# Kernel tuning notes

Hardware: AMD Instinct MI355X
Metric: run time of the kernel (lower is better)

Reference implementation:

```python
import jax, jax.numpy as jnp
import numpy as np

EPS_FEAT = 1e-4   # stabilizer eps inside favorp_projection
EPS_DEN = 0.01    # clamp_min eps for the attention denominator


def favorp_projection(data, projection_matrix, is_query):
    # data: [b, h, n, d]; projection_matrix: [h, m, d]
    d = data.shape[-1]
    data_normalizer = d ** (-0.25)
    ratio = projection_matrix.shape[1] ** (-0.5)
    data_dash = jnp.einsum('bhnd,hmd->bhnm', data_normalizer * data, projection_matrix)
    diag_data = (jnp.sum(data * data, axis=-1) * 0.5 * data_normalizer * data_normalizer)[..., None]
    if is_query:
        stabilizer = jax.lax.stop_gradient(jnp.max(data_dash, axis=-1, keepdims=True))
    else:
        stabilizer = jax.lax.stop_gradient(jnp.max(data_dash, axis=(-1, -2), keepdims=True))
    return ratio * jnp.exp(data_dash - diag_data - stabilizer) + EPS_FEAT


def setup_inputs() -> dict:
    key = jax.random.key(0)
    ks = jax.random.split(key, 12)
    N, B, E, H, D, M = 4096, 4, 1024, 16, 64, 64
    s = E ** -0.5
    return {
        'query': jax.random.normal(ks[0], (N, B, E), jnp.float32),
        'key': jax.random.normal(ks[1], (N, B, E), jnp.float32),
        'value': jax.random.normal(ks[2], (N, B, E), jnp.float32),
        'Wq': jax.random.normal(ks[3], (E, E), jnp.float32) * s,
        'bq': jax.random.normal(ks[4], (E,), jnp.float32) * 0.02,
        'Wk': jax.random.normal(ks[5], (E, E), jnp.float32) * s,
        'bk': jax.random.normal(ks[6], (E,), jnp.float32) * 0.02,
        'Wv': jax.random.normal(ks[7], (E, E), jnp.float32) * s,
        'bv': jax.random.normal(ks[8], (E,), jnp.float32) * 0.02,
        'Wo': jax.random.normal(ks[9], (E, E), jnp.float32) * s,
        'bo': jax.random.normal(ks[10], (E,), jnp.float32) * 0.02,
        'proj': jax.random.normal(ks[11], (H, M, D), jnp.float32),
    }


def reference(query, key, value, Wq, bq, Wk, bk, Wv, bv, Wo, bo, proj):
    H = proj.shape[0]
    # [n, b, e] -> [b, n, e]
    q_in = query.transpose(1, 0, 2)
    k_in = key.transpose(1, 0, 2)
    v_in = value.transpose(1, 0, 2)
    B, N, E = q_in.shape
    D = E // H

    def lin(x, W, b):
        return jnp.einsum('bne,fe->bnf', x, W) + b

    def split_heads(x):  # [b, n, e] -> [b, h, n, d]
        return x.reshape(B, N, H, D).transpose(0, 2, 1, 3)

    q = split_heads(lin(q_in, Wq, bq))
    k = split_heads(lin(k_in, Wk, bk))
    v = split_heads(lin(v_in, Wv, bv))

    q_prime = favorp_projection(q, proj, is_query=True)   # [b, h, n, m]
    k_prime = favorp_projection(k, proj, is_query=False)  # [b, h, n, m]

    # non-causal linear attention: O(n * m * d)
    kv = jnp.einsum('bhnm,bhnd->bhmd', k_prime, v)
    qkv = jnp.einsum('bhnm,bhmd->bhnd', q_prime, kv)
    normalizer = jnp.einsum('bhnm,bhm->bhn', q_prime, k_prime.sum(axis=2))
    output = qkv / jnp.maximum(normalizer[..., None], EPS_DEN)

    attn_output = output.transpose(0, 2, 1, 3).reshape(B, N, E)  # b h n d -> b n (h d)
    out = lin(attn_output, Wo, bo)
    return out.transpose(1, 0, 2)  # back to [n, b, e]
```

## Files before the change

kernel.cpp:

```cpp
#include <hip/hip_runtime.h>
#include <math.h>

#define B_   4
#define N_   4096
#define E_   1024
#define H_   16
#define BN_  (B_*N_)
#define BH_  (B_*H_)
#define SPLITK 8

#define NRM_C   0.35355339059327373f
#define DIAG_C  0.0625f
#define RATIO_C 0.125f
#define EPSF    1e-4f
#define EPSD    0.01f

typedef __attribute__((ext_vector_type(8))) short bf16x8;
typedef __attribute__((ext_vector_type(4))) float f32x4;

__device__ __forceinline__ unsigned short f32_to_bf16(float x) {
    unsigned int u = __float_as_uint(x);
    unsigned int r = (u + 0x7fffu + ((u >> 16) & 1u)) >> 16;
    return (unsigned short)r;
}
__device__ __forceinline__ float bf16_to_f32(unsigned short h) {
    return __uint_as_float(((unsigned int)h) << 16);
}

__device__ __forceinline__ unsigned int pk_bf16(float a, float b) {
    unsigned int r;
    asm("v_cvt_pk_bf16_f32 %0, %1, %2" : "=v"(r) : "v"(a), "v"(b));
    return r;
}

__device__ __forceinline__ void f32x8_split(float4 fa, float4 fb, bf16x8& hi, bf16x8& lo) {
    unsigned int h0 = pk_bf16(fa.x, fa.y), h1 = pk_bf16(fa.z, fa.w);
    unsigned int h2 = pk_bf16(fb.x, fb.y), h3 = pk_bf16(fb.z, fb.w);
    float e0 = __uint_as_float(h0 << 16), e1 = __uint_as_float(h0 & 0xffff0000u);
    float e2 = __uint_as_float(h1 << 16), e3 = __uint_as_float(h1 & 0xffff0000u);
    float e4 = __uint_as_float(h2 << 16), e5 = __uint_as_float(h2 & 0xffff0000u);
    float e6 = __uint_as_float(h3 << 16), e7 = __uint_as_float(h3 & 0xffff0000u);
    unsigned int l0 = pk_bf16(fa.x - e0, fa.y - e1), l1 = pk_bf16(fa.z - e2, fa.w - e3);
    unsigned int l2 = pk_bf16(fb.x - e4, fb.y - e5), l3 = pk_bf16(fb.z - e6, fb.w - e7);
    union { unsigned int u[4]; bf16x8 v; } H, L;
    H.u[0] = h0; H.u[1] = h1; H.u[2] = h2; H.u[3] = h3;
    L.u[0] = l0; L.u[1] = l1; L.u[2] = l2; L.u[3] = l3;
    hi = H.v; lo = L.v;
}

__device__ __forceinline__ void atomicMaxF(float* addr, float v) {
    if (v >= 0.f) atomicMax((int*)addr, __float_as_int(v));
    else          atomicMin((unsigned int*)addr, __float_as_uint(v));
}

__global__ void init_stab(float* stab) {
    if (threadIdx.x < BH_) stab[threadIdx.x] = -INFINITY;
}

template<int IN_MODE>
__global__ __launch_bounds__(256) void convert_split(const float* __restrict__ src,
                                                     unsigned short* __restrict__ hi,
                                                     unsigned short* __restrict__ lo,
                                                     int total4)
{
    int i = blockIdx.x * 256 + threadIdx.x;
    const int stride = gridDim.x * 256;
    for (; i < total4; i += stride) {
        long e4 = (long)i * 4;
        const float* p;
        if (IN_MODE == 0) {
            long r = e4 >> 10; int e = (int)(e4 & 1023);
            int b = (int)(r >> 12), n = (int)(r & 4095);
            p = src + (((long)(n * B_ + b)) << 10) + e;
        } else {
            p = src + e4;
        }
        float4 v = *(const float4*)p;
        ushort4 h, l;
        h.x = f32_to_bf16(v.x); l.x = f32_to_bf16(v.x - bf16_to_f32(h.x));
        h.y = f32_to_bf16(v.y); l.y = f32_to_bf16(v.y - bf16_to_f32(h.y));
        h.z = f32_to_bf16(v.z); l.z = f32_to_bf16(v.z - bf16_to_f32(h.z));
        h.w = f32_to_bf16(v.w); l.w = f32_to_bf16(v.w - bf16_to_f32(h.w));
        *(ushort4*)(hi + e4) = h;
        *(ushort4*)(lo + e4) = l;
    }
}

__device__ __forceinline__ void gl_lds16(const unsigned short* g, unsigned short* l) {
    __builtin_amdgcn_global_load_lds((const __attribute__((address_space(1))) void*)g,
                                     (__attribute__((address_space(3))) void*)l, 16, 0, 0);
}

#define SMEM_BYTES (4*64*68*4 + 2*4*64*4)

template<int MODE>
__global__ __launch_bounds__(256) void gemm_mfma(const unsigned short* __restrict__ Ahi,
                                                 const unsigned short* __restrict__ Alo,
                                                 const unsigned short* __restrict__ Bhi,
                                                 const unsigned short* __restrict__ Blo,
                                                 const float* __restrict__ bias,
                                                 float* __restrict__ Y,
                                                 float* __restrict__ stab,
                                                 const unsigned short* __restrict__ PShi,
                                                 const unsigned short* __restrict__ PSlo,
                                                 const unsigned short* __restrict__ kvThi,
                                                 const unsigned short* __restrict__ kvTlo,
                                                 const float* __restrict__ ksum,
                                                 unsigned short* __restrict__ AttnHi,
                                                 unsigned short* __restrict__ AttnLo)
{
    __shared__ __align__(16) char SMEM[SMEM_BYTES];
    unsigned short* smem = (unsigned short*)SMEM;
    const int t = threadIdx.x;
    const int w = t >> 6, lane = t & 63;
    const int row0 = blockIdx.x * 128, col0 = blockIdx.y * 128;
    const int wrow = (w >> 1) * 64, wcol = (w & 1) * 64;
    const int g = lane >> 4, rl = lane & 15;
    const int lr8 = lane >> 3, lc8 = lane & 7;

    const int sr = w * 32 + (lane >> 2);
    const int kswz = (((lane & 3) ^ ((lane >> 2) & 3)) << 3);
    const long aoff = (long)(row0 + sr) * E_ + kswz;
    const long boff = (long)(col0 + sr) * E_ + kswz;

    f32x4 acc[4][4];
#pragma unroll
    for (int m = 0; m < 4; ++m)
#pragma unroll
        for (int n = 0; n < 4; ++n) acc[m][n] = (f32x4){0.f, 0.f, 0.f, 0.f};

#define STAGE_STEP(KS, BUF)                                                          \
    {                                                                                \
        const int k0 = (KS) * 32;                                                    \
        unsigned short* d = smem + (BUF) * 16384 + w * 1024;                         \
        gl_lds16(Ahi + aoff + k0,             d);                                    \
        gl_lds16(Ahi + aoff + k0 + 16 * E_,   d + 512);                              \
        gl_lds16(Alo + aoff + k0,             d + 4096);                             \
        gl_lds16(Alo + aoff + k0 + 16 * E_,   d + 4096 + 512);                       \
        gl_lds16(Bhi + boff + k0,             d + 8192);                             \
        gl_lds16(Bhi + boff + k0 + 16 * E_,   d + 8192 + 512);                       \
        gl_lds16(Blo + boff + k0,             d + 12288);                            \
        gl_lds16(Blo + boff + k0 + 16 * E_,   d + 12288 + 512);                      \
    }

    STAGE_STEP(0, 0);

    for (int ks = 0; ks < 32; ++ks) {
        __syncthreads();
        if (ks + 1 < 32) STAGE_STEP(ks + 1, (ks + 1) & 1);
        const unsigned short* sb = smem + (ks & 1) * 16384;
        bf16x8 ah[4], al[4], bh[4], bl[4];
#pragma unroll
        for (int m = 0; m < 4; ++m) {
            int r = wrow + m * 16 + rl;
            int off = r * 32 + ((g ^ (r & 3)) << 3);
            ah[m] = *(const bf16x8*)(sb + off);
            al[m] = *(const bf16x8*)(sb + 4096 + off);
        }
#pragma unroll
        for (int n = 0; n < 4; ++n) {
            int r = wcol + n * 16 + rl;
            int off = r * 32 + ((g ^ (r & 3)) << 3);
            bh[n] = *(const bf16x8*)(sb + 8192 + off);
            bl[n] = *(const bf16x8*)(sb + 12288 + off);
        }
#pragma unroll
        for (int m = 0; m < 4; ++m)
#pragma unroll
            for (int n = 0; n < 4; ++n)
                acc[m][n] = __builtin_amdgcn_mfma_f32_16x16x32_bf16(ah[m], bh[n], acc[m][n], 0, 0, 0);
#pragma unroll
        for (int m = 0; m < 4; ++m)
#pragma unroll
            for (int n = 0; n < 4; ++n)
                acc[m][n] = __builtin_amdgcn_mfma_f32_16x16x32_bf16(ah[m], bl[n], acc[m][n], 0, 0, 0);
#pragma unroll
        for (int m = 0; m < 4; ++m)
#pragma unroll
            for (int n = 0; n < 4; ++n)
                acc[m][n] = __builtin_amdgcn_mfma_f32_16x16x32_bf16(al[m], bh[n], acc[m][n], 0, 0, 0);
    }
#undef STAGE_STEP

    float bv[4];
#pragma unroll
    for (int n = 0; n < 4; ++n) bv[n] = bias[col0 + wcol + n * 16 + rl];

    if (MODE <= 1) {
#pragma unroll
        for (int m = 0; m < 4; ++m) {
            int rbase = row0 + wrow + m * 16 + g * 4;
#pragma unroll
            for (int n = 0; n < 4; ++n) {
                int c = col0 + wcol + n * 16 + rl;
#pragma unroll
                for (int q = 0; q < 4; ++q) {
                    int r = rbase + q;
                    float v = acc[m][n][q] + bv[n];
                    long off;
                    if (MODE == 0) off = (long)r * E_ + c;
                    else { int b = r >> 12, nn = r & (N_ - 1); off = (long)(nn * B_ + b) * E_ + c; }
                    Y[off] = v;
                }
            }
        }
        return;
    }

    __syncthreads();
    float* accF  = (float*)SMEM + w * (64 * 68);
    float* diagL = (float*)(SMEM + 4*64*68*4) + w * 64;
    float* rnmL  = (float*)(SMEM + 4*64*68*4) + 256 + w * 64;
    const int b_idx = row0 >> 12;
    const int hg = (col0 >> 6) + (w & 1);
    const int bh_i = b_idx * H_ + hg;

    bf16x8 pbh[8], pbl[8];
#pragma unroll
    for (int n = 0; n < 4; ++n)
#pragma unroll
        for (int kk = 0; kk < 2; ++kk) {
            long po = (long)hg * 4096 + (n*16 + rl) * 64 + kk*32 + g*8;
            pbh[n*2+kk] = *(const bf16x8*)(PShi + po);
            pbl[n*2+kk] = *(const bf16x8*)(PSlo + po);
        }

#pragma unroll
    for (int m = 0; m < 4; ++m)
#pragma unroll
        for (int n = 0; n < 4; ++n)
#pragma unroll
            for (int q = 0; q < 4; ++q)
                accF[(m*16 + g*4 + q) * 68 + n*16 + rl] = acc[m][n][q] + bv[n];
    {
        float s = 0.f;
#pragma unroll 16
        for (int d = 0; d < 64; ++d) { float x = accF[lane * 68 + d]; s = fmaf(x, x, s); }
        diagL[lane] = s * DIAG_C;
    }
    __syncthreads();

    float wavemax = -INFINITY;
#pragma unroll
    for (int mi = 0; mi < 4; ++mi) {
        bf16x8 dah[2], dal[2];
#pragma unroll
        for (int kk = 0; kk < 2; ++kk) {
            const float* src = &accF[(mi*16 + rl) * 68 + kk*32 + g*8];
            float4 f0 = *(const float4*)src, f1 = *(const float4*)(src + 4);
            f32x8_split(f0, f1, dah[kk], dal[kk]);
        }
        f32x4 dacc[4];
#pragma unroll
        for (int n = 0; n < 4; ++n) dacc[n] = (f32x4){0.f,0.f,0.f,0.f};
#pragma unroll
        for (int n = 0; n < 4; ++n)
#pragma unroll
            for (int kk = 0; kk < 2; ++kk) {
                dacc[n] = __builtin_amdgcn_mfma_f32_16x16x32_bf16(dah[kk], pbh[n*2+kk], dacc[n], 0, 0, 0);
                dacc[n] = __builtin_amdgcn_mfma_f32_16x16x32_bf16(dah[kk], pbl[n*2+kk], dacc[n], 0, 0, 0);
                dacc[n] = __builtin_amdgcn_mfma_f32_16x16x32_bf16(dal[kk], pbh[n*2+kk], dacc[n], 0, 0, 0);
            }
        if (MODE == 2) {
#pragma unroll
            for (int n = 0; n < 4; ++n)
#pragma unroll
                for (int q = 0; q < 4; ++q) {
                    float dsh = dacc[n][q] * NRM_C;
                    wavemax = fmaxf(wavemax, dsh);
                    int rloc = mi*16 + g*4 + q;
                    accF[rloc * 68 + n*16 + rl] = dsh - diagL[rloc];
                }
        } else {
            float rm0 = -INFINITY, rm1 = -INFINITY, rm2 = -INFINITY, rm3 = -INFINITY;
#pragma unroll
            for (int n = 0; n < 4; ++n) {
                rm0 = fmaxf(rm0, dacc[n][0]); rm1 = fmaxf(rm1, dacc[n][1]);
                rm2 = fmaxf(rm2, dacc[n][2]); rm3 = fmaxf(rm3, dacc[n][3]);
            }
#pragma unroll
            for (int off = 1; off < 16; off <<= 1) {
                rm0 = fmaxf(rm0, __shfl_xor(rm0, off));
                rm1 = fmaxf(rm1, __shfl_xor(rm1, off));
                rm2 = fmaxf(rm2, __shfl_xor(rm2, off));
                rm3 = fmaxf(rm3, __shfl_xor(rm3, off));
            }
            float rmq[4] = {rm0 * NRM_C, rm1 * NRM_C, rm2 * NRM_C, rm3 * NRM_C};
#pragma unroll
            for (int n = 0; n < 4; ++n)
#pragma unroll
                for (int q = 0; q < 4; ++q) {
                    int rloc = mi*16 + g*4 + q;
                    float qp = RATIO_C * expf(dacc[n][q] * NRM_C - diagL[rloc] - rmq[q]) + EPSF;
                    accF[rloc * 68 + n*16 + rl] = qp;
                }
        }
    }

    if (MODE == 2) {
#pragma unroll
        for (int off = 1; off < 64; off <<= 1) wavemax = fmaxf(wavemax, __shfl_xor(wavemax, off));
        if (lane == 0) atomicMaxF(&stab[bh_i], wavemax);
#pragma unroll
        for (int pass = 0; pass < 8; ++pass) {
            int rloc = pass * 8 + lr8;
            const float* sp = &accF[rloc * 68 + lc8 * 8];
            float4 f0 = *(const float4*)sp;
            float4 f1 = *(const float4*)(sp + 4);
            long off = (long)(row0 + wrow + rloc) * E_ + col0 + wcol + lc8 * 8;
            *(float4*)(Y + off) = f0;
            *(float4*)(Y + off + 4) = f1;
        }
        return;
    }

    {
        float s = 0.f;
        const float* kb = ksum + bh_i * 64;
#pragma unroll 16
        for (int m = 0; m < 64; ++m) s = fmaf(accF[lane * 68 + m], kb[m], s);
        rnmL[lane] = 1.f / fmaxf(s, EPSD);
    }
    bf16x8 kbh[8], kbl[8];
#pragma unroll
    for (int n = 0; n < 4; ++n)
#pragma unroll
        for (int kk = 0; kk < 2; ++kk) {
            long ko = (long)bh_i * 4096 + (n*16 + rl) * 64 + kk*32 + g*8;
            kbh[n*2+kk] = *(const bf16x8*)(kvThi + ko);
            kbl[n*2+kk] = *(const bf16x8*)(kvTlo + ko);
        }
    __syncthreads();
#pragma unroll
    for (int mi = 0; mi < 4; ++mi) {
        bf16x8 qah[2], qal[2];
#pragma unroll
        for (int kk = 0; kk < 2; ++kk) {
            const float* src = &accF[(mi*16 + rl) * 68 + kk*32 + g*8];
            float4 f0 = *(const float4*)src, f1 = *(const float4*)(src + 4);
            f32x8_split(f0, f1, qah[kk], qal[kk]);
        }
        f32x4 oacc[4];
#pragma unroll
        for (int n = 0; n < 4; ++n) oacc[n] = (f32x4){0.f,0.f,0.f,0.f};
#pragma unroll
        for (int n = 0; n < 4; ++n)
#pragma unroll
            for (int kk = 0; kk < 2; ++kk) {
                oacc[n] = __builtin_amdgcn_mfma_f32_16x16x32_bf16(qah[kk], kbh[n*2+kk], oacc[n], 0, 0, 0);
                oacc[n] = __builtin_amdgcn_mfma_f32_16x16x32_bf16(qah[kk], kbl[n*2+kk], oacc[n], 0, 0, 0);
                oacc[n] = __builtin_amdgcn_mfma_f32_16x16x32_bf16(qal[kk], kbh[n*2+kk], oacc[n], 0, 0, 0);
            }
#pragma unroll
        for (int n = 0; n < 4; ++n)
#pragma unroll
            for (int q = 0; q < 4; ++q) {
                int rloc = mi*16 + g*4 + q;
                accF[rloc * 68 + n*16 + rl] = oacc[n][q] * rnmL[rloc];
            }
    }
#pragma unroll
    for (int pass = 0; pass < 8; ++pass) {
        int rloc = pass * 8 + lr8;
        const float* sp = &accF[rloc * 68 + lc8 * 8];
        float4 f0 = *(const float4*)sp;
        float4 f1 = *(const float4*)(sp + 4);
        float v[8] = {f0.x,f0.y,f0.z,f0.w,f1.x,f1.y,f1.z,f1.w};
        unsigned int hu[4], lu[4];
#pragma unroll
        for (int j = 0; j < 4; ++j) {
            hu[j] = pk_bf16(v[2*j], v[2*j+1]);
            float ea = __uint_as_float(hu[j] << 16);
            float eb = __uint_as_float(hu[j] & 0xffff0000u);
            lu[j] = pk_bf16(v[2*j] - ea, v[2*j+1] - eb);
        }
        long off = (long)(row0 + wrow + rloc) * E_ + col0 + wcol + lc8 * 8;
        uint4 hv = {hu[0], hu[1], hu[2], hu[3]};
        uint4 lv = {lu[0], lu[1], lu[2], lu[3]};
        *(uint4*)(AttnHi + off) = hv;
        *(uint4*)(AttnLo + off) = lv;
    }
}

template<int IN_MODE, int OUT_MODE>
__global__ __launch_bounds__(256) void lin_gemm(const float* __restrict__ X,
                                                const float* __restrict__ W,
                                                const float* __restrict__ bias,
                                                float* __restrict__ Y)
{
    __shared__ float As[16][68];
    __shared__ float Ws[16][68];
    const int row0 = blockIdx.x * 64;
    const int col0 = blockIdx.y * 64;
    const int t  = threadIdx.x;
    const int lr = t >> 2;
    const int lk = (t & 3) * 4;
    const int ty = t >> 4, tx = t & 15;

    long arow;
    {
        int r = row0 + lr;
        if (IN_MODE == 0) { int b = r >> 12, n = r & (N_ - 1); arow = (long)(n * B_ + b) * E_; }
        else              { arow = (long)r * E_; }
    }
    const long wrow = (long)(col0 + lr) * E_;

    float acc[4][4] = {};
    for (int e0 = 0; e0 < E_; e0 += 16) {
        float4 av = *(const float4*)(X + arow + e0 + lk);
        float4 wv = *(const float4*)(W + wrow + e0 + lk);
        As[lk+0][lr] = av.x; As[lk+1][lr] = av.y; As[lk+2][lr] = av.z; As[lk+3][lr] = av.w;
        Ws[lk+0][lr] = wv.x; Ws[lk+1][lr] = wv.y; Ws[lk+2][lr] = wv.z; Ws[lk+3][lr] = wv.w;
        __syncthreads();
#pragma unroll
        for (int k = 0; k < 16; ++k) {
            float4 a = *(const float4*)&As[k][ty*4];
            float4 w = *(const float4*)&Ws[k][tx*4];
            float a_[4] = {a.x,a.y,a.z,a.w};
            float w_[4] = {w.x,w.y,w.z,w.w};
#pragma unroll
            for (int i = 0; i < 4; ++i)
#pragma unroll
                for (int j = 0; j < 4; ++j)
                    acc[i][j] = fmaf(a_[i], w_[j], acc[i][j]);
        }
        __syncthreads();
    }
    float4 bvv = *(const float4*)(bias + col0 + tx*4);
    float b_[4] = {bvv.x,bvv.y,bvv.z,bvv.w};
#pragma unroll
    for (int i = 0; i < 4; ++i) {
        int r = row0 + ty*4 + i;
        float4 o;
        o.x = acc[i][0] + b_[0]; o.y = acc[i][1] + b_[1];
        o.z = acc[i][2] + b_[2]; o.w = acc[i][3] + b_[3];
        long off;
        if (OUT_MODE == 0) off = (long)r * E_ + col0 + tx*4;
        else { int b = r >> 12, n = r & (N_ - 1); off = (long)(n * B_ + b) * E_ + col0 + tx*4; }
        *(float4*)(Y + off) = o;
    }
}

template<int IS_QUERY>
__global__ __launch_bounds__(256) void favorp_dash(float* __restrict__ Xh,
                                                   const float* __restrict__ proj,
                                                   float* __restrict__ stab)
{
    __shared__ float Xs[64][68];
    __shared__ float Ps[64][68];
    __shared__ float diag[64];
    __shared__ float red4[4];
    __shared__ float rowred[64][17];
    const int bh = blockIdx.x, b = bh >> 4, h = bh & 15;
    const int n0 = blockIdx.y * 64;
    const int t = threadIdx.x;
    const int r = t >> 2, c0 = (t & 3) * 16;
    const int ty = t >> 4, tx = t & 15;

    const float* xrow = Xh + (long)(b * N_ + n0 + r) * E_ + h * 64;
    const float* prow = proj + (long)(h * 64 + r) * 64;
#pragma unroll
    for (int c = 0; c < 4; ++c) {
        float4 v = *(const float4*)(xrow + c0 + c*4);
        Xs[c0+c*4+0][r] = v.x; Xs[c0+c*4+1][r] = v.y; Xs[c0+c*4+2][r] = v.z; Xs[c0+c*4+3][r] = v.w;
        float4 p = *(const float4*)(prow + c0 + c*4);
        Ps[c0+c*4+0][r] = p.x; Ps[c0+c*4+1][r] = p.y; Ps[c0+c*4+2][r] = p.z; Ps[c0+c*4+3][r] = p.w;
    }
    __syncthreads();
    if (t < 64) {
        float s = 0.f;
#pragma unroll 16
        for (int d = 0; d < 64; ++d) { float x = Xs[d][t]; s = fmaf(x, x, s); }
        diag[t] = s * DIAG_C;
    }
    __syncthreads();

    float acc[4][4] = {};
#pragma unroll 16
    for (int d = 0; d < 64; ++d) {
        float4 a = *(const float4*)&Xs[d][ty*4];
        float4 p = *(const float4*)&Ps[d][tx*4];
        float a_[4] = {a.x,a.y,a.z,a.w};
        float p_[4] = {p.x,p.y,p.z,p.w};
#pragma unroll
        for (int i = 0; i < 4; ++i)
#pragma unroll
            for (int j = 0; j < 4; ++j)
                acc[i][j] = fmaf(a_[i], p_[j], acc[i][j]);
    }
    float dash[4][4];
#pragma unroll
    for (int i = 0; i < 4; ++i)
#pragma unroll
        for (int j = 0; j < 4; ++j) dash[i][j] = acc[i][j] * NRM_C;

    if (IS_QUERY) {
#pragma unroll
        for (int i = 0; i < 4; ++i) {
            float m = fmaxf(fmaxf(dash[i][0], dash[i][1]), fmaxf(dash[i][2], dash[i][3]));
            rowred[ty*4+i][tx] = m;
        }
        __syncthreads();
#pragma unroll
        for (int i = 0; i < 4; ++i) {
            int row = ty*4 + i;
            float m = rowred[row][0];
#pragma unroll
            for (int jj = 1; jj < 16; ++jj) m = fmaxf(m, rowred[row][jj]);
            float dg = diag[row];
            float4 o;
            o.x = RATIO_C * expf(dash[i][0] - dg - m) + EPSF;
            o.y = RATIO_C * expf(dash[i][1] - dg - m) + EPSF;
            o.z = RATIO_C * expf(dash[i][2] - dg - m) + EPSF;
            o.w = RATIO_C * expf(dash[i][3] - dg - m) + EPSF;
            *(float4*)(Xh + (long)(b * N_ + n0 + row) * E_ + h * 64 + tx*4) = o;
        }
    } else {
        float lmax = dash[0][0];
#pragma unroll
        for (int i = 0; i < 4; ++i)
#pragma unroll
            for (int j = 0; j < 4; ++j) lmax = fmaxf(lmax, dash[i][j]);
#pragma unroll
        for (int i = 0; i < 4; ++i) {
            int row = ty*4 + i;
            float dg = diag[row];
            float4 o = { dash[i][0]-dg, dash[i][1]-dg, dash[i][2]-dg, dash[i][3]-dg };
            *(float4*)(Xh + (long)(b * N_ + n0 + row) * E_ + h * 64 + tx*4) = o;
        }
#pragma unroll
        for (int off = 32; off > 0; off >>= 1) lmax = fmaxf(lmax, __shfl_down(lmax, off));
        if ((t & 63) == 0) red4[t >> 6] = lmax;
        __syncthreads();
        if (t == 0)
            atomicMaxF(&stab[bh], fmaxf(fmaxf(red4[0], red4[1]), fmaxf(red4[2], red4[3])));
    }
}

__global__ __launch_bounds__(256) void kv_partial(const float* __restrict__ T1,
                                                  const float* __restrict__ V,
                                                  const float* __restrict__ stab,
                                                  float* __restrict__ kvp,
                                                  float* __restrict__ ksump)
{
    __shared__ float KPs[16][68];
    __shared__ float Vs[16][68];
    const int bh = blockIdx.x, chunk = blockIdx.y;
    const int b = bh >> 4, h = bh & 15;
    const int t = threadIdx.x;
    const int lr = t >> 4, lm = (t & 15) * 4;
    const int ty = t >> 4, tx = t & 15;
    const float stb = stab[bh];
    float acc[4][4] = {};
    float ks = 0.f;
    const int nbeg = chunk * (N_ / SPLITK), nend = nbeg + (N_ / SPLITK);
    for (int n0 = nbeg; n0 < nend; n0 += 16) {
        long rowoff = (long)(b * N_ + n0 + lr) * E_ + h * 64 + lm;
        float4 tv = *(const float4*)(T1 + rowoff);
        float4 vv = *(const float4*)(V + rowoff);
        KPs[lr][lm+0] = RATIO_C * expf(tv.x - stb) + EPSF;
        KPs[lr][lm+1] = RATIO_C * expf(tv.y - stb) + EPSF;
        KPs[lr][lm+2] = RATIO_C * expf(tv.z - stb) + EPSF;
        KPs[lr][lm+3] = RATIO_C * expf(tv.w - stb) + EPSF;
        *(float4*)&Vs[lr][lm] = vv;
        __syncthreads();
        if (t < 64) {
#pragma unroll
            for (int rr = 0; rr < 16; ++rr) ks += KPs[rr][t];
        }
#pragma unroll
        for (int k = 0; k < 16; ++k) {
            float4 a = *(const float4*)&KPs[k][ty*4];
            float4 v4 = *(const float4*)&Vs[k][tx*4];
            float a_[4] = {a.x,a.y,a.z,a.w};
            float v_[4] = {v4.x,v4.y,v4.z,v4.w};
#pragma unroll
            for (int i = 0; i < 4; ++i)
#pragma unroll
                for (int j = 0; j < 4; ++j)
                    acc[i][j] = fmaf(a_[i], v_[j], acc[i][j]);
        }
        __syncthreads();
    }
    const long kvbase = ((long)chunk * BH_ + bh) * 4096;
#pragma unroll
    for (int i = 0; i < 4; ++i) {
        float4 o = {acc[i][0], acc[i][1], acc[i][2], acc[i][3]};
        *(float4*)(kvp + kvbase + (ty*4+i) * 64 + tx*4) = o;
    }
    if (t < 64) ksump[((long)chunk * BH_ + bh) * 64 + t] = ks;
}

__global__ __launch_bounds__(256) void kv_reduce(const float* __restrict__ kvp,
                                                 const float* __restrict__ ksump,
                                                 float* __restrict__ kvM,
                                                 float* __restrict__ ksum,
                                                 unsigned short* __restrict__ kvThi,
                                                 unsigned short* __restrict__ kvTlo)
{
    int idx = blockIdx.x * 256 + threadIdx.x;
    if (idx < BH_ * 4096) {
        float s = 0.f;
#pragma unroll
        for (int c = 0; c < SPLITK; ++c) s += kvp[(long)c * BH_ * 4096 + idx];
        kvM[idx] = s;
        int bh = idx >> 12, md = idx & 4095, m = md >> 6, d = md & 63;
        unsigned short h16 = f32_to_bf16(s);
        long toff = (long)bh * 4096 + d * 64 + m;
        kvThi[toff] = h16;
        kvTlo[toff] = f32_to_bf16(s - bf16_to_f32(h16));
    } else {
        int j = idx - BH_ * 4096;
        if (j < BH_ * 64) {
            float s = 0.f;
#pragma unroll
            for (int c = 0; c < SPLITK; ++c) s += ksump[(long)c * BH_ * 64 + j];
            ksum[j] = s;
        }
    }
}

__global__ __launch_bounds__(256) void qkv_attn(const float* __restrict__ Qp,
                                                const float* __restrict__ kvM,
                                                const float* __restrict__ ksum,
                                                float* __restrict__ attn)
{
    __shared__ float QPs[64][68];
    __shared__ float kvs[64][68];
    __shared__ float ksums[64];
    __shared__ float rnorm[64];
    const int bh = blockIdx.x, b = bh >> 4, h = bh & 15;
    const int n0 = blockIdx.y * 64;
    const int t = threadIdx.x;
    const int r = t >> 2, c0 = (t & 3) * 16;
    const int ty = t >> 4, tx = t & 15;

#pragma unroll
    for (int c = 0; c < 4; ++c) {
        int idx = t * 16 + c * 4;
        float4 v = *(const float4*)(kvM + (long)bh * 4096 + idx);
        *(float4*)&kvs[idx >> 6][idx & 63] = v;
    }
    if (t < 64) ksums[t] = ksum[bh * 64 + t];
    const float* qrow = Qp + (long)(b * N_ + n0 + r) * E_ + h * 64;
#pragma unroll
    for (int c = 0; c < 4; ++c) {
        float4 v = *(const float4*)(qrow + c0 + c*4);
        QPs[c0+c*4+0][r] = v.x; QPs[c0+c*4+1][r] = v.y; QPs[c0+c*4+2][r] = v.z; QPs[c0+c*4+3][r] = v.w;
    }
    __syncthreads();
    if (t < 64) {
        float s = 0.f;
#pragma unroll 16
        for (int m = 0; m < 64; ++m) s = fmaf(QPs[m][t], ksums[m], s);
        rnorm[t] = 1.f / fmaxf(s, EPSD);
    }
    __syncthreads();
    float acc[4][4] = {};
#pragma unroll 16
    for (int m = 0; m < 64; ++m) {
        float4 a = *(const float4*)&QPs[m][ty*4];
        float4 v4 = *(const float4*)&kvs[m][tx*4];
        float a_[4] = {a.x,a.y,a.z,a.w};
        float v_[4] = {v4.x,v4.y,v4.z,v4.w};
#pragma unroll
        for (int i = 0; i < 4; ++i)
#pragma unroll
            for (int j = 0; j < 4; ++j)
                acc[i][j] = fmaf(a_[i], v_[j], acc[i][j]);
    }
#pragma unroll
    for (int i = 0; i < 4; ++i) {
        int row = ty*4 + i;
        float rn = rnorm[row];
        float4 o = {acc[i][0]*rn, acc[i][1]*rn, acc[i][2]*rn, acc[i][3]*rn};
        *(float4*)(attn + (long)(b * N_ + n0 + row) * E_ + h * 64 + tx*4) = o;
    }
}

extern "C" void kernel_launch(void* const* d_in, const int* in_sizes, int n_in,
                              void* d_out, int out_size, void* d_ws, size_t ws_size,
                              hipStream_t stream)
{
    const float* query = (const float*)d_in[0];
    const float* key   = (const float*)d_in[1];
    const float* value = (const float*)d_in[2];
    const float* Wq    = (const float*)d_in[3];
    const float* bq    = (const float*)d_in[4];
    const float* Wk    = (const float*)d_in[5];
    const float* bk    = (const float*)d_in[6];
    const float* Wv    = (const float*)d_in[7];
    const float* bv    = (const float*)d_in[8];
    const float* Wo    = (const float*)d_in[9];
    const float* bo    = (const float*)d_in[10];
    const float* proj  = (const float*)d_in[11];
    float* O = (float*)d_out;

    float* ws = (float*)d_ws;
    const size_t SZ = (size_t)BN_ * E_;
    float* A     = ws;
    float* kvp   = ws + SZ;
    float* ksump = kvp + (size_t)SPLITK * BH_ * 4096;
    float* kvM   = ksump + (size_t)SPLITK * BH_ * 64;
    float* ksum  = kvM + (size_t)BH_ * 4096;
    float* stab  = ksum + (size_t)BH_ * 64;
    unsigned short* kvThi = (unsigned short*)(stab + 64);
    unsigned short* kvTlo = kvThi + (size_t)BH_ * 4096;
    unsigned short* PShi  = kvTlo + (size_t)BH_ * 4096;
    unsigned short* PSlo  = PShi + 65536;
    const size_t EXTRA_F = (size_t)BH_ * 4096  + 65536 ;
    const size_t COMMON_F = SZ + (size_t)SPLITK * BH_ * 4096 + (size_t)SPLITK * BH_ * 64
                          + (size_t)BH_ * 4096 + (size_t)BH_ * 64 + 64 + EXTRA_F;
    unsigned short* Xhi = (unsigned short*)(ws + COMMON_F);
    unsigned short* Xlo = Xhi + SZ;
    unsigned short* Whi = Xlo + SZ;
    unsigned short* Wlo = Whi + (size_t)E_ * E_;
    const size_t NEED_FAST = (COMMON_F + SZ + (size_t)E_ * E_) * 4;

    dim3 gF(BH_, N_ / 64);
    dim3 gKV(BH_, SPLITK);
    const int nRed = (BH_ * 4096 + BH_ * 64) / 256;

    if (ws_size >= NEED_FAST) {
        dim3 gG(BN_ / 128, E_ / 128);
        const int X4 = (int)(SZ / 4), W4 = (E_ * E_) / 4;
        unsigned short* AttnHi = (unsigned short*)A;
        unsigned short* AttnLo = AttnHi + SZ;

        convert_split<1><<<64, 256, 0, stream>>>(proj, PShi, PSlo, 16384);
        init_stab<<<1, 64, 0, stream>>>(stab);
        convert_split<0><<<2048, 256, 0, stream>>>(key, Xhi, Xlo, X4);
        convert_split<1><<<1024, 256, 0, stream>>>(Wk, Whi, Wlo, W4);
        gemm_mfma<2><<<gG, 256, 0, stream>>>(Xhi, Xlo, Whi, Wlo, bk, O, stab,
                                             PShi, PSlo, nullptr, nullptr, nullptr, nullptr, nullptr);
        convert_split<0><<<2048, 256, 0, stream>>>(value, Xhi, Xlo, X4);
        convert_split<1><<<1024, 256, 0, stream>>>(Wv, Whi, Wlo, W4);
        gemm_mfma<0><<<gG, 256, 0, stream>>>(Xhi, Xlo, Whi, Wlo, bv, A, nullptr,
                                             nullptr, nullptr, nullptr, nullptr, nullptr, nullptr, nullptr);
        kv_partial<<<gKV, 256, 0, stream>>>(O, A, stab, kvp, ksump);
        kv_reduce<<<nRed, 256, 0, stream>>>(kvp, ksump, kvM, ksum, kvThi, kvTlo);
        convert_split<0><<<2048, 256, 0, stream>>>(query, Xhi, Xlo, X4);
        convert_split<1><<<1024, 256, 0, stream>>>(Wq, Whi, Wlo, W4);
        gemm_mfma<3><<<gG, 256, 0, stream>>>(Xhi, Xlo, Whi, Wlo, bq, nullptr, nullptr,
                                             PShi, PSlo, kvThi, kvTlo, ksum, AttnHi, AttnLo);
        convert_split<1><<<1024, 256, 0, stream>>>(Wo, Whi, Wlo, W4);
        gemm_mfma<1><<<gG, 256, 0, stream>>>(AttnHi, AttnLo, Whi, Wlo, bo, O, nullptr,
                                             nullptr, nullptr, nullptr, nullptr, nullptr, nullptr, nullptr);
    } else {
        dim3 gGemm(BN_ / 64, E_ / 64);
        lin_gemm<0,0><<<gGemm, 256, 0, stream>>>(key, Wk, bk, O);
        init_stab<<<1, 64, 0, stream>>>(stab);
        favorp_dash<0><<<gF, 256, 0, stream>>>(O, proj, stab);
        lin_gemm<0,0><<<gGemm, 256, 0, stream>>>(value, Wv, bv, A);
        kv_partial<<<gKV, 256, 0, stream>>>(O, A, stab, kvp, ksump);
        kv_reduce<<<nRed, 256, 0, stream>>>(kvp, ksump, kvM, ksum, kvThi, kvTlo);
        lin_gemm<0,0><<<gGemm, 256, 0, stream>>>(query, Wq, bq, O);
        favorp_dash<1><<<gF, 256, 0, stream>>>(O, proj, stab);
        qkv_attn<<<gF, 256, 0, stream>>>(O, kvM, ksum, A);
        lin_gemm<1,1><<<gGemm, 256, 0, stream>>>(A, Wo, bo, O);
    }
}
```

Before: 593.9 us.

## Add 8-wave triple-buffered GEMM for value and output projections

Adds a new 512-thread GEMM kernel with 256x128 tiles and a three-stage LDS ring fed by direct global-to-LDS loads. Loads for the next stages are interleaved between MFMA sub-blocks, and setprio raises wave priority during the MFMA bursts. The new kernel replaces the plain GEMM modes (V projection and output projection), and the now-unused plain-store epilogue is dropped from the old kernel. The aim is better overlap of memory traffic with MFMA work and more data reuse per tile. The cost is large dynamic LDS (144KB) and many barriers per k-step, which could limit occupancy.

```diff
diff --git a/kernel.cpp b/kernel.cpp
--- a/kernel.cpp
+++ b/kernel.cpp
@@ -89,6 +89,192 @@
 __device__ __forceinline__ void gl_lds16(const unsigned short* g, unsigned short* l) {
     __builtin_amdgcn_global_load_lds((const __attribute__((address_space(1))) void*)g,
                                      (__attribute__((address_space(3))) void*)l, 16, 0, 0);
+}
+
+#define SMEM_DYN8 147456
+
+template<int MODE>
+__global__ __launch_bounds__(512, 2) void gemm8p(const unsigned short* __restrict__ Ahi,
+                                                 const unsigned short* __restrict__ Alo,
+                                                 const unsigned short* __restrict__ Bhi,
+                                                 const unsigned short* __restrict__ Blo,
+                                                 const float* __restrict__ bias,
+                                                 float* __restrict__ Y)
+{
+    extern __shared__ char SMEM8[];
+    unsigned short* U = (unsigned short*)SMEM8;
+    const int t = threadIdx.x;
+    const int w = t >> 6, lane = t & 63;
+    const int row0 = blockIdx.x * 256, col0 = blockIdx.y * 128;
+    const int wrow = (w >> 1) * 64, wcol = (w & 1) * 64;
+    const int g = lane >> 4, rl = lane & 15;
+
+    int gi0 = t, gi1 = 512 + t;
+    int ar0 = gi0 >> 2, as0 = gi0 & 3;
+    int ar1 = gi1 >> 2, as1 = gi1 & 3;
+    const long aSrc0 = (long)(row0 + ar0) * E_ + ((as0 ^ (ar0 & 3)) << 3);
+    const long aSrc1 = (long)(row0 + ar1) * E_ + ((as1 ^ (ar1 & 3)) << 3);
+    const int aDst0 = (w * 64) * 8;
+    const int aDst1 = (512 + w * 64) * 8;
+    const long bSrc = (long)(col0 + (t >> 2)) * E_ + (((t & 3) ^ ((t >> 2) & 3)) << 3);
+    const int bDst = (w * 64) * 8;
+
+    f32x4 acc[4][4];
+#pragma unroll
+    for (int m = 0; m < 4; ++m)
+#pragma unroll
+        for (int n = 0; n < 4; ++n) acc[m][n] = (f32x4){0.f, 0.f, 0.f, 0.f};
+
+#define STAGE_FULL(TILE, BUFI) {                                        \
+        const int k0_ = (TILE) * 32;                                    \
+        unsigned short* bu_ = U + (BUFI) * 24576;                       \
+        gl_lds16(Ahi + aSrc0 + k0_, bu_ + aDst0);                       \
+        gl_lds16(Ahi + aSrc1 + k0_, bu_ + aDst1);                       \
+        gl_lds16(Alo + aSrc0 + k0_, bu_ + 8192 + aDst0);                \
+        gl_lds16(Alo + aSrc1 + k0_, bu_ + 8192 + aDst1);                \
+        gl_lds16(Bhi + bSrc + k0_, bu_ + 16384 + bDst);                 \
+        gl_lds16(Blo + bSrc + k0_, bu_ + 20480 + bDst); }
+
+    STAGE_FULL(0, 0);
+    STAGE_FULL(1, 1);
+    asm volatile("s_waitcnt vmcnt(6)" ::: "memory");
+    __builtin_amdgcn_s_barrier();
+    __builtin_amdgcn_sched_barrier(0);
+
+    for (int tt = 0; tt < 32; ++tt) {
+        const unsigned short* sb = U + (tt % 3) * 24576;
+        unsigned short* ub = U + ((tt + 2) % 3) * 24576;
+        const bool st = (tt + 2 < 32);
+        const int k2 = (tt + 2) * 32;
+        bf16x8 bhf[4], blf[4];
+
+#pragma unroll
+        for (int n = 0; n < 4; ++n) {
+            int r = wcol + n * 16 + rl;
+            int off = r * 32 + ((g ^ (r & 3)) << 3);
+            bhf[n] = *(const bf16x8*)(sb + 16384 + off);
+            blf[n] = *(const bf16x8*)(sb + 20480 + off);
+        }
+        {
+            int r = wrow + rl;
+            int off = r * 32 + ((g ^ (r & 3)) << 3);
+            bf16x8 ah = *(const bf16x8*)(sb + off);
+            bf16x8 al = *(const bf16x8*)(sb + 8192 + off);
+            if (st) { gl_lds16(Ahi + aSrc0 + k2, ub + aDst0);
+                      gl_lds16(Ahi + aSrc1 + k2, ub + aDst1); }
+            asm volatile("s_waitcnt lgkmcnt(0)" ::: "memory");
+            __builtin_amdgcn_sched_barrier(0);
+            __builtin_amdgcn_s_setprio(1);
+#pragma unroll
+            for (int n = 0; n < 4; ++n)
+                acc[0][n] = __builtin_amdgcn_mfma_f32_16x16x32_bf16(ah, bhf[n], acc[0][n], 0, 0, 0);
+#pragma unroll
+            for (int n = 0; n < 4; ++n)
+                acc[0][n] = __builtin_amdgcn_mfma_f32_16x16x32_bf16(ah, blf[n], acc[0][n], 0, 0, 0);
+#pragma unroll
+            for (int n = 0; n < 4; ++n)
+                acc[0][n] = __builtin_amdgcn_mfma_f32_16x16x32_bf16(al, bhf[n], acc[0][n], 0, 0, 0);
+            __builtin_amdgcn_s_setprio(0);
+        }
+        __builtin_amdgcn_s_barrier();
+        __builtin_amdgcn_sched_barrier(0);
+
+        {
+            int r = wrow + 16 + rl;
+            int off = r * 32 + ((g ^ (r & 3)) << 3);
+            bf16x8 ah = *(const bf16x8*)(sb + off);
+            bf16x8 al = *(const bf16x8*)(sb + 8192 + off);
+            if (st) { gl_lds16(Alo + aSrc0 + k2, ub + 8192 + aDst0);
+                      gl_lds16(Alo + aSrc1 + k2, ub + 8192 + aDst1); }
+            asm volatile("s_waitcnt lgkmcnt(0)" ::: "memory");
+            __builtin_amdgcn_sched_barrier(0);
+            __builtin_amdgcn_s_setprio(1);
+#pragma unroll
+            for (int n = 0; n < 4; ++n)
+                acc[1][n] = __builtin_amdgcn_mfma_f32_16x16x32_bf16(ah, bhf[n], acc[1][n], 0, 0, 0);
+#pragma unroll
+            for (int n = 0; n < 4; ++n)
+                acc[1][n] = __builtin_amdgcn_mfma_f32_16x16x32_bf16(ah, blf[n], acc[1][n], 0, 0, 0);
+#pragma unroll
+            for (int n = 0; n < 4; ++n)
+                acc[1][n] = __builtin_amdgcn_mfma_f32_16x16x32_bf16(al, bhf[n], acc[1][n], 0, 0, 0);
+            __builtin_amdgcn_s_setprio(0);
+        }
+        __builtin_amdgcn_s_barrier();
+        __builtin_amdgcn_sched_barrier(0);
+
+        {
+            int r = wrow + 32 + rl;
+            int off = r * 32 + ((g ^ (r & 3)) << 3);
+            bf16x8 ah = *(const bf16x8*)(sb + off);
+            bf16x8 al = *(const bf16x8*)(sb + 8192 + off);
+            if (st) gl_lds16(Bhi + bSrc + k2, ub + 16384 + bDst);
+            asm volatile("s_waitcnt lgkmcnt(0)" ::: "memory");
+            __builtin_amdgcn_sched_barrier(0);
+            __builtin_amdgcn_s_setprio(1);
+#pragma unroll
+            for (int n = 0; n < 4; ++n)
+                acc[2][n] = __builtin_amdgcn_mfma_f32_16x16x32_bf16(ah, bhf[n], acc[2][n], 0, 0, 0);
+#pragma unroll
+            for (int n = 0; n < 4; ++n)
+                acc[2][n] = __builtin_amdgcn_mfma_f32_16x16x32_bf16(ah, blf[n], acc[2][n], 0, 0, 0);
+#pragma unroll
+            for (int n = 0; n < 4; ++n)
+                acc[2][n] = __builtin_amdgcn_mfma_f32_16x16x32_bf16(al, bhf[n], acc[2][n], 0, 0, 0);
+            __builtin_amdgcn_s_setprio(0);
+        }
+        __builtin_amdgcn_s_barrier();
+        __builtin_amdgcn_sched_barrier(0);
+
+        {
+            int r = wrow + 48 + rl;
+            int off = r * 32 + ((g ^ (r & 3)) << 3);
+            bf16x8 ah = *(const bf16x8*)(sb + off);
+            bf16x8 al = *(const bf16x8*)(sb + 8192 + off);
+            if (st) gl_lds16(Blo + bSrc + k2, ub + 20480 + bDst);
+            asm volatile("s_waitcnt lgkmcnt(0)" ::: "memory");
+            __builtin_amdgcn_sched_barrier(0);
+            __builtin_amdgcn_s_setprio(1);
+#pragma unroll
+            for (int n = 0; n < 4; ++n)
+                acc[3][n] = __builtin_amdgcn_mfma_f32_16x16x32_bf16(ah, bhf[n], acc[3][n], 0, 0, 0);
+#pragma unroll
+            for (int n = 0; n < 4; ++n)
+                acc[3][n] = __builtin_amdgcn_mfma_f32_16x16x32_bf16(ah, blf[n], acc[3][n], 0, 0, 0);
+#pragma unroll
+            for (int n = 0; n < 4; ++n)
+                acc[3][n] = __builtin_amdgcn_mfma_f32_16x16x32_bf16(al, bhf[n], acc[3][n], 0, 0, 0);
+            __builtin_amdgcn_s_setprio(0);
+        }
+        if (tt < 31) {
+            if (st) asm volatile("s_waitcnt vmcnt(6)" ::: "memory");
+            else    asm volatile("s_waitcnt vmcnt(0)" ::: "memory");
+            __builtin_amdgcn_s_barrier();
+            __builtin_amdgcn_sched_barrier(0);
+        }
+    }
+#undef STAGE_FULL
+
+    float bv[4];
+#pragma unroll
+    for (int n = 0; n < 4; ++n) bv[n] = bias[col0 + wcol + n * 16 + rl];
+#pragma unroll
+    for (int m = 0; m < 4; ++m) {
+        int rbase = row0 + wrow + m * 16 + g * 4;
+#pragma unroll
+        for (int n = 0; n < 4; ++n) {
+            int c = col0 + wcol + n * 16 + rl;
+#pragma unroll
+            for (int q = 0; q < 4; ++q) {
+                int r = rbase + q;
+                float v = acc[m][n][q] + bv[n];
+                long off;
+                if (MODE == 0) off = (long)r * E_ + c;
+                else { int b = r >> 12, nn = r & (N_ - 1); off = (long)(nn * B_ + b) * E_ + c; }
+                Y[off] = v;
+            }
+        }
+    }
 }
 
 #define SMEM_BYTES (4*64*68*4 + 2*4*64*4)
@@ -185,27 +371,6 @@
     float bv[4];
 #pragma unroll
     for (int n = 0; n < 4; ++n) bv[n] = bias[col0 + wcol + n * 16 + rl];
-
-    if (MODE <= 1) {
-#pragma unroll
-        for (int m = 0; m < 4; ++m) {
-            int rbase = row0 + wrow + m * 16 + g * 4;
-#pragma unroll
-            for (int n = 0; n < 4; ++n) {
-                int c = col0 + wcol + n * 16 + rl;
-#pragma unroll
-                for (int q = 0; q < 4; ++q) {
-                    int r = rbase + q;
-                    float v = acc[m][n][q] + bv[n];
-                    long off;
-                    if (MODE == 0) off = (long)r * E_ + c;
-                    else { int b = r >> 12, nn = r & (N_ - 1); off = (long)(nn * B_ + b) * E_ + c; }
-                    Y[off] = v;
-                }
-            }
-        }
-        return;
-    }
 
     __syncthreads();
     float* accF  = (float*)SMEM + w * (64 * 68);
@@ -723,9 +888,13 @@
 
     if (ws_size >= NEED_FAST) {
         dim3 gG(BN_ / 128, E_ / 128);
+        dim3 gP(BN_ / 256, E_ / 128);
         const int X4 = (int)(SZ / 4), W4 = (E_ * E_) / 4;
         unsigned short* AttnHi = (unsigned short*)A;
         unsigned short* AttnLo = AttnHi + SZ;
+
+        (void)hipFuncSetAttribute((const void*)&gemm8p<0>, hipFuncAttributeMaxDynamicSharedMemorySize, SMEM_DYN8);
+        (void)hipFuncSetAttribute((const void*)&gemm8p<1>, hipFuncAttributeMaxDynamicSharedMemorySize, SMEM_DYN8);
 
         convert_split<1><<<64, 256, 0, stream>>>(proj, PShi, PSlo, 16384);
         init_stab<<<1, 64, 0, stream>>>(stab);
@@ -735,8 +904,7 @@
                                              PShi, PSlo, nullptr, nullptr, nullptr, nullptr, nullptr);
         convert_split<0><<<2048, 256, 0, stream>>>(value, Xhi, Xlo, X4);
         convert_split<1><<<1024, 256, 0, stream>>>(Wv, Whi, Wlo, W4);
-        gemm_mfma<0><<<gG, 256, 0, stream>>>(Xhi, Xlo, Whi, Wlo, bv, A, nullptr,
-                                             nullptr, nullptr, nullptr, nullptr, nullptr, nullptr, nullptr);
+        gemm8p<0><<<gP, 512, SMEM_DYN8, stream>>>(Xhi, Xlo, Whi, Wlo, bv, A);
         kv_partial<<<gKV, 256, 0, stream>>>(O, A, stab, kvp, ksump);
         kv_reduce<<<nRed, 256, 0, stream>>>(kvp, ksump, kvM, ksum, kvThi, kvTlo);
         convert_split<0><<<2048, 256, 0, stream>>>(query, Xhi, Xlo, X4);
@@ -744,8 +912,7 @@
         gemm_mfma<3><<<gG, 256, 0, stream>>>(Xhi, Xlo, Whi, Wlo, bq, nullptr, nullptr,
                                              PShi, PSlo, kvThi, kvTlo, ksum, AttnHi, AttnLo);
         convert_split<1><<<1024, 256, 0, stream>>>(Wo, Whi, Wlo, W4);
-        gemm_mfma<1><<<gG, 256, 0, stream>>>(AttnHi, AttnLo, Whi, Wlo, bo, O, nullptr,
-                                             nullptr, nullptr, nullptr, nullptr, nullptr, nullptr, nullptr);
+        gemm8p<1><<<gP, 512, SMEM_DYN8, stream>>>(AttnHi, AttnLo, Whi, Wlo, bo, O);
     } else {
         dim3 gGemm(BN_ / 64, E_ / 64);
         lin_gemm<0,0><<<gGemm, 256, 0, stream>>>(key, Wk, bk, O);
```

After: 588.1 us. No clear change (-1.0%).
